# Performance work log

Measured on AMD Instinct MI355X. Metric: run time of the kernel, lower is better.

Reference implementation:

```python
import jax, jax.numpy as jnp
import numpy as np

NEG_SLOPE = 0.01  # torch leaky_relu default

def _lrelu(x):
    return jax.nn.leaky_relu(x, NEG_SLOPE)

def _l2norm(x, axis):
    # torch F.normalize(p=2, eps=1e-12)
    n = jnp.linalg.norm(x, axis=axis, keepdims=True)
    return x / jnp.maximum(n, 1e-12)

def setup_inputs() -> dict:
    key = jax.random.key(0)
    ks = jax.random.split(key, 12)
    Nda, Nq, C, Din, Dout = 10000, 64, 1024, 128, 256
    target_adj = (jax.random.uniform(ks[0], (Nda, Nda)) < 0.002).astype(jnp.float32)
    query_adj = (jax.random.uniform(ks[1], (Nq, Nq)) < 0.2).astype(jnp.float32)
    node_features_da = jax.random.normal(ks[2], (Nda, Din), dtype=jnp.float32)
    node_features_q = jax.random.normal(ks[3], (Nq, Din), dtype=jnp.float32)
    candidate_set = jax.random.randint(ks[4], (C,), 0, Nda)
    candidate_adj = (jax.random.uniform(ks[5], (C, C)) < 0.01).astype(jnp.float32)
    s_in = 1.0 / np.sqrt(Din).astype(np.float32)
    s_out = 1.0 / np.sqrt(Dout).astype(np.float32)
    W1_da = jax.random.normal(ks[6], (Din, Dout), dtype=jnp.float32) * s_in
    W1_q = jax.random.normal(ks[7], (Din, Dout), dtype=jnp.float32) * s_in
    W2_da = jax.random.normal(ks[8], (Dout, Dout), dtype=jnp.float32) * s_out
    W2_q = jax.random.normal(ks[9], (Dout, Dout), dtype=jnp.float32) * s_out
    threshold = jnp.float32(0.2)
    return {"target_adj": target_adj, "node_features_da": node_features_da,
            "query_adj": query_adj, "node_features_q": node_features_q,
            "candidate_set": candidate_set, "candidate_adj": candidate_adj,
            "threshold": threshold, "W1_da": W1_da, "W1_q": W1_q,
            "W2_da": W2_da, "W2_q": W2_q}

def _cross_cosine(q, da, candidate_set):
    # cosine similarity between each query node and each candidate target node: [Nq, C]
    return _l2norm(q, 1) @ _l2norm(da[candidate_set], 1).T

def reference(target_adj, node_features_da, query_adj, node_features_q,
              candidate_set, candidate_adj, threshold, W1_da, W1_q, W2_da, W2_q):
    # layer 1: GCN propagation on both graphs (gcn(adj,x) = adj @ x @ W)
    da1 = _lrelu(target_adj @ (node_features_da @ W1_da))   # [Nda, D]
    q1 = _lrelu(query_adj @ (node_features_q @ W1_q))       # [Nq, D]
    c1 = _cross_cosine(q1, da1, candidate_set)               # [Nq, C]
    pre_da1 = da1[candidate_set]                             # [C, D]
    # NOTE: da1[candidate_set].data = ... mutates a temporary in torch -> no-op on da1
    att_da1 = _lrelu(da1)                                    # dropout in eval = identity
    h1_q = c1 @ pre_da1                                      # [Nq, D]
    att_q1 = _lrelu(q1 + _l2norm(h1_q, 0))
    # layer 2
    da2 = _lrelu(target_adj @ (att_da1 @ W2_da))
    q2 = _lrelu(query_adj @ (att_q1 @ W2_q))
    c2 = _cross_cosine(q2, da2, candidate_set)
    pre_da2 = da2[candidate_set]
    att_da2 = _lrelu(da2)                                    # in-place update is again a no-op
    h2_q = c2 @ pre_da2
    att_q2 = _lrelu(q2 + _l2norm(h2_q, 0))
    # graph-level matching score per target node
    emb = jnp.mean(att_q2, axis=0, keepdims=True)            # [1, D]
    num = att_da2 @ emb[0]                                   # [Nda]
    den = jnp.maximum(jnp.linalg.norm(att_da2, axis=1) * jnp.linalg.norm(emb), 1e-8)
    end = (num / den)[None, :]                               # [1, Nda]
    # threshold selection expressed with a mask (jit-safe, same math: excluded
    # rows/cols are zero and do not affect L2 norms, sums, or the trace)
    m = (end[0] > threshold).astype(att_da2.dtype)           # [Nda]
    F_ = att_da2 * m[:, None]
    re_adj = F_ @ F_.T                                       # [Nda, Nda]
    nor_re = _l2norm(re_adj, 1) * target_adj                 # elementwise with original adj
    cnt = jnp.sum(m)
    total = jnp.sum(nor_re)
    tr = jnp.trace(nor_re)
    has = cnt > 0
    pre_avg_degree = jnp.where(has, total / jnp.maximum(cnt, 1.0), 0.0)
    pre_avg_nodes = jnp.where(has, tr, 0.0)
    pre_density = jnp.where(has, 2.0 * total / (tr * (tr - 1.0) + 1e-4), 0.0)
    return (end, att_da2, att_q2, pre_avg_degree, pre_density, pre_avg_nodes)
```

## Files before the change

kernel.cpp:

```cpp
#include <hip/hip_runtime.h>

constexpr int NDA = 10000;
constexpr int NQ  = 64;
constexpr int CND = 1024;
constexpr int DIN = 128;
constexpr int D   = 256;
constexpr int CAP = 96;
constexpr int NT128 = (NDA + 127) / 128;
constexpr int NB128 = NT128 * 2;
constexpr int NCHUNK = 32;
constexpr int GCHUNK = 320;

#define LRELU(x) ((x) >= 0.f ? (x) : 0.01f * (x))

__device__ __forceinline__ float wave_red64(float v) {
#pragma unroll
    for (int o = 32; o; o >>= 1) v += __shfl_down(v, o);
    return v;
}

struct GemmSmem    { float As[32][65]; float Bs[32][68]; };
struct Gemm128Smem { float As[16][132]; float Bs[16][132]; };
struct CrossSmem   { float qs[D]; float cmw[256]; int sci[256]; float red[4]; float sqn; float part[4][256]; };
struct SpmmSmem    { int sc[CAP]; float part[4][256]; };
struct CsrSmem     { int scnt; };
struct EndSmem     { float se[D]; float scnt; float red[4]; };
struct FinalSmem   { int sc[CAP]; float part[4][256]; int n; int sdiag; float r1[4], r2[4], r3[4]; };
struct Attq4Smem   { float hbuf[64][65]; float red[4][64]; float invs[64]; };

template <bool RELU_A, bool RELU_C>
__device__ __forceinline__ void gemm_body(GemmSmem& sm, int bx, int by,
                                          const float* __restrict__ A,
                                          const float* __restrict__ B,
                                          float* __restrict__ C,
                                          int M, int N, int K) {
    const int bm = bx * 64, bn = by * 64;
    const int tid = threadIdx.x;
    const int tx = tid & 15, ty = tid >> 4;
    const int lm = tid >> 2, lk = (tid & 3) * 8;
    const int kb = tid >> 3, nb = (tid & 7) * 8;
    const bool aValid = (bm + lm) < M;
    const float* aPtr = A + (size_t)(bm + lm) * K + lk;
    const float* bPtr = B + (size_t)kb * N + bn + nb;
    float4 ra0 = make_float4(0.f, 0.f, 0.f, 0.f), ra1 = ra0, rb0, rb1;
    if (aValid) { ra0 = *(const float4*)aPtr; ra1 = *(const float4*)(aPtr + 4); }
    rb0 = *(const float4*)bPtr;
    rb1 = *(const float4*)(bPtr + 4);
    float acc[4][4] = {};
    for (int k0 = 0; k0 < K; k0 += 32) {
        float4 wa0 = ra0, wa1 = ra1, wb0 = rb0, wb1 = rb1;
        if (RELU_A) {
            wa0.x = LRELU(wa0.x); wa0.y = LRELU(wa0.y); wa0.z = LRELU(wa0.z); wa0.w = LRELU(wa0.w);
            wa1.x = LRELU(wa1.x); wa1.y = LRELU(wa1.y); wa1.z = LRELU(wa1.z); wa1.w = LRELU(wa1.w);
        }
        sm.As[lk + 0][lm] = wa0.x; sm.As[lk + 1][lm] = wa0.y;
        sm.As[lk + 2][lm] = wa0.z; sm.As[lk + 3][lm] = wa0.w;
        sm.As[lk + 4][lm] = wa1.x; sm.As[lk + 5][lm] = wa1.y;
        sm.As[lk + 6][lm] = wa1.z; sm.As[lk + 7][lm] = wa1.w;
        *(float4*)&sm.Bs[kb][nb]     = wb0;
        *(float4*)&sm.Bs[kb][nb + 4] = wb1;
        __syncthreads();
        if (k0 + 32 < K) {
            if (aValid) {
                ra0 = *(const float4*)(aPtr + k0 + 32);
                ra1 = *(const float4*)(aPtr + k0 + 36);
            }
            rb0 = *(const float4*)(bPtr + (size_t)(k0 + 32) * N);
            rb1 = *(const float4*)(bPtr + (size_t)(k0 + 32) * N + 4);
        }
#pragma unroll
        for (int kk = 0; kk < 32; kk++) {
            float av[4], bv[4];
#pragma unroll
            for (int i = 0; i < 4; i++) av[i] = sm.As[kk][ty * 4 + i];
#pragma unroll
            for (int j = 0; j < 4; j++) bv[j] = sm.Bs[kk][tx * 4 + j];
#pragma unroll
            for (int i = 0; i < 4; i++)
#pragma unroll
                for (int j = 0; j < 4; j++) acc[i][j] += av[i] * bv[j];
        }
        __syncthreads();
    }
#pragma unroll
    for (int i = 0; i < 4; i++) {
        int r = bm + ty * 4 + i;
        if (r < M) {
            float4 v = make_float4(acc[i][0], acc[i][1], acc[i][2], acc[i][3]);
            if (RELU_C) { v.x = LRELU(v.x); v.y = LRELU(v.y); v.z = LRELU(v.z); v.w = LRELU(v.w); }
            *(float4*)(C + (size_t)r * N + bn + tx * 4) = v;
        }
    }
}

template <bool RELU_A>
__device__ __forceinline__ void gemm128_body(Gemm128Smem& sm, int bx, int by,
                                             const float* __restrict__ A,
                                             const float* __restrict__ B,
                                             float* __restrict__ C,
                                             int M, int N, int K) {
    const int bm = bx * 128, bn = by * 128;
    const int tid = threadIdx.x;
    const int tx = tid & 15, ty = tid >> 4;
    const int am = tid >> 1, ak = (tid & 1) * 8;
    const int bk = tid >> 4, bn8 = (tid & 15) * 8;
    const bool aValid = (bm + am) < M;
    const float* aPtr = A + (size_t)(bm + am) * K + ak;
    const float* bPtr = B + (size_t)bk * N + bn + bn8;
    float4 ra0 = make_float4(0.f, 0.f, 0.f, 0.f), ra1 = ra0, rb0, rb1;
    if (aValid) { ra0 = *(const float4*)aPtr; ra1 = *(const float4*)(aPtr + 4); }
    rb0 = *(const float4*)bPtr;
    rb1 = *(const float4*)(bPtr + 4);
    float acc[8][8] = {};
    for (int k0 = 0; k0 < K; k0 += 16) {
        float a8[8] = { ra0.x, ra0.y, ra0.z, ra0.w, ra1.x, ra1.y, ra1.z, ra1.w };
        if (RELU_A) {
#pragma unroll
            for (int j = 0; j < 8; j++) a8[j] = LRELU(a8[j]);
        }
#pragma unroll
        for (int j = 0; j < 8; j++) sm.As[ak + j][am] = a8[j];
        *(float4*)&sm.Bs[bk][bn8]     = rb0;
        *(float4*)&sm.Bs[bk][bn8 + 4] = rb1;
        __syncthreads();
        if (k0 + 16 < K) {
            if (aValid) {
                ra0 = *(const float4*)(aPtr + k0 + 16);
                ra1 = *(const float4*)(aPtr + k0 + 20);
            }
            rb0 = *(const float4*)(bPtr + (size_t)(k0 + 16) * N);
            rb1 = *(const float4*)(bPtr + (size_t)(k0 + 16) * N + 4);
        }
#pragma unroll
        for (int kk = 0; kk < 16; kk++) {
            float4 a0 = *(const float4*)&sm.As[kk][ty * 8];
            float4 a1 = *(const float4*)&sm.As[kk][ty * 8 + 4];
            float4 b0 = *(const float4*)&sm.Bs[kk][tx * 8];
            float4 b1 = *(const float4*)&sm.Bs[kk][tx * 8 + 4];
            float av[8] = { a0.x, a0.y, a0.z, a0.w, a1.x, a1.y, a1.z, a1.w };
            float bv[8] = { b0.x, b0.y, b0.z, b0.w, b1.x, b1.y, b1.z, b1.w };
#pragma unroll
            for (int i = 0; i < 8; i++)
#pragma unroll
                for (int j = 0; j < 8; j++) acc[i][j] += av[i] * bv[j];
        }
        __syncthreads();
    }
#pragma unroll
    for (int i = 0; i < 8; i++) {
        int r = bm + ty * 8 + i;
        if (r < M) {
            float4 v0 = make_float4(acc[i][0], acc[i][1], acc[i][2], acc[i][3]);
            float4 v1 = make_float4(acc[i][4], acc[i][5], acc[i][6], acc[i][7]);
            *(float4*)(C + (size_t)r * N + bn + tx * 8)     = v0;
            *(float4*)(C + (size_t)r * N + bn + tx * 8 + 4) = v1;
        }
    }
}

__device__ __forceinline__ void csr_body(CsrSmem& sm, const float* __restrict__ adj,
                                         int* __restrict__ cols,
                                         int* __restrict__ rowcnt, int row) {
    if (threadIdx.x == 0) sm.scnt = 0;
    __syncthreads();
    const float4* rp = (const float4*)(adj + (size_t)row * NDA);
    for (int i = threadIdx.x; i < NDA / 4; i += 256) {
        float4 v = rp[i];
        if (v.x != 0.f) { int s = atomicAdd(&sm.scnt, 1); if (s < CAP) cols[row * CAP + s] = 4 * i; }
        if (v.y != 0.f) { int s = atomicAdd(&sm.scnt, 1); if (s < CAP) cols[row * CAP + s] = 4 * i + 1; }
        if (v.z != 0.f) { int s = atomicAdd(&sm.scnt, 1); if (s < CAP) cols[row * CAP + s] = 4 * i + 2; }
        if (v.w != 0.f) { int s = atomicAdd(&sm.scnt, 1); if (s < CAP) cols[row * CAP + s] = 4 * i + 3; }
    }
    __syncthreads();
    if (threadIdx.x == 0) rowcnt[row] = min(sm.scnt, CAP);
}

__device__ __forceinline__ void spmm_body(SpmmSmem& sm, const int* __restrict__ cols,
                                          const int* __restrict__ rowcnt,
                                          const float* __restrict__ X,
                                          float* __restrict__ out1,
                                          float* __restrict__ out2, int row) {
    int t = threadIdx.x;
    int w = t >> 6, lane = t & 63;
    int cnt = rowcnt[row];
    if (t < cnt) sm.sc[t] = cols[row * CAP + t];
    __syncthreads();
    float4 acc = make_float4(0.f, 0.f, 0.f, 0.f);
    int k = w;
    for (; k + 4 < cnt; k += 8) {
        const float4* x0 = (const float4*)(X + (size_t)sm.sc[k] * D);
        const float4* x1 = (const float4*)(X + (size_t)sm.sc[k + 4] * D);
        float4 v0 = x0[lane];
        float4 v1 = x1[lane];
        acc.x += v0.x + v1.x; acc.y += v0.y + v1.y;
        acc.z += v0.z + v1.z; acc.w += v0.w + v1.w;
    }
    for (; k < cnt; k += 4) {
        const float4* x0 = (const float4*)(X + (size_t)sm.sc[k] * D);
        float4 v0 = x0[lane];
        acc.x += v0.x; acc.y += v0.y; acc.z += v0.z; acc.w += v0.w;
    }
    *(float4*)&sm.part[w][lane * 4] = acc;
    __syncthreads();
    float s = sm.part[0][t] + sm.part[1][t] + sm.part[2][t] + sm.part[3][t];
    float v = LRELU(s);
    out1[(size_t)row * D + t] = v;
    if (out2) out2[(size_t)row * D + t] = LRELU(v);
}

__device__ __forceinline__ void cross_body(CrossSmem& sm, const float* __restrict__ q,
                                           const float* __restrict__ da,
                                           const int* __restrict__ cand,
                                           float* __restrict__ hpart,
                                           int r, int qr) {
    int t = threadIdx.x;
    int w = t >> 6, lane = t & 63;
    float qv = q[r * D + t];
    sm.qs[t] = qv;
    sm.sci[t] = cand[qr * 256 + t];
    float p = wave_red64(qv * qv);
    if (lane == 0) sm.red[w] = p;
    __syncthreads();
    if (t == 0) sm.sqn = fmaxf(sqrtf(sm.red[0] + sm.red[1] + sm.red[2] + sm.red[3]), 1e-12f);
    __syncthreads();
    float qn = sm.sqn;
    float4 qv4 = *(const float4*)&sm.qs[lane * 4];
    for (int c = w * 64; c < w * 64 + 64; c++) {
        const float4* rp = (const float4*)(da + (size_t)sm.sci[c] * D);
        float4 v = rp[lane];
        float dp = qv4.x * v.x + qv4.y * v.y + qv4.z * v.z + qv4.w * v.w;
        float sq = v.x * v.x + v.y * v.y + v.z * v.z + v.w * v.w;
#pragma unroll
        for (int o = 32; o; o >>= 1) { dp += __shfl_down(dp, o); sq += __shfl_down(sq, o); }
        if (lane == 0) sm.cmw[c] = dp / (qn * fmaxf(sqrtf(sq), 1e-12f));
    }
    __syncthreads();
    float4 acc = make_float4(0.f, 0.f, 0.f, 0.f);
    for (int c = w; c < 256; c += 8) {
        float w0 = sm.cmw[c], w1 = sm.cmw[c + 4];
        const float4* p0 = (const float4*)(da + (size_t)sm.sci[c] * D);
        const float4* p1 = (const float4*)(da + (size_t)sm.sci[c + 4] * D);
        float4 v0 = p0[lane];
        float4 v1 = p1[lane];
        acc.x += w0 * v0.x + w1 * v1.x;
        acc.y += w0 * v0.y + w1 * v1.y;
        acc.z += w0 * v0.z + w1 * v1.z;
        acc.w += w0 * v0.w + w1 * v1.w;
    }
    *(float4*)&sm.part[w][lane * 4] = acc;
    __syncthreads();
    float hs = sm.part[0][t] + sm.part[1][t] + sm.part[2][t] + sm.part[3][t];
    hpart[((size_t)qr * NQ + r) * D + t] = hs;
}

__global__ __launch_bounds__(256) void stage0_kernel(const float* __restrict__ adj,
                                                     int* __restrict__ cols,
                                                     int* __restrict__ rowcnt,
                                                     const float* __restrict__ Fda,
                                                     const float* __restrict__ W1da,
                                                     float* __restrict__ X1,
                                                     const float* __restrict__ Fq,
                                                     const float* __restrict__ W1q,
                                                     float* __restrict__ Xq) {
    __shared__ union { Gemm128Smem h; GemmSmem g; CsrSmem z; } sm;
    int bid = blockIdx.x;
    if (bid < NB128) {
        gemm128_body<false>(sm.h, bid >> 1, bid & 1, Fda, W1da, X1, NDA, D, DIN);
    } else if (bid < NB128 + 4) {
        gemm_body<false, false>(sm.g, 0, bid - NB128, Fq, W1q, Xq, NQ, D, DIN);
    } else {
        csr_body(sm.z, adj, cols, rowcnt, bid - (NB128 + 4));
    }
}

__global__ __launch_bounds__(256) void stage_sg_kernel(const int* __restrict__ cols,
                                                       const int* __restrict__ rowcnt,
                                                       const float* __restrict__ X,
                                                       float* __restrict__ out1,
                                                       float* __restrict__ out2,
                                                       const float* __restrict__ Aq,
                                                       const float* __restrict__ Bq,
                                                       float* __restrict__ Cq) {
    __shared__ union { GemmSmem g; SpmmSmem s; } sm;
    int bid = blockIdx.x;
    if (bid < 4) {
        gemm_body<false, true>(sm.g, 0, bid, Aq, Bq, Cq, NQ, D, NQ);
    } else {
        spmm_body(sm.s, cols, rowcnt, X, out1, out2, bid - 4);
    }
}

__global__ __launch_bounds__(256) void mergeA_kernel(const float* __restrict__ q1,
                                                     const float* __restrict__ da1,
                                                     const int* __restrict__ cand,
                                                     float* __restrict__ hpart,
                                                     const float* __restrict__ W2da,
                                                     float* __restrict__ Y2) {
    __shared__ union { CrossSmem c; Gemm128Smem h; } sm;
    int bid = blockIdx.x;
    if (bid < 256) {
        cross_body(sm.c, q1, da1, cand, hpart, bid >> 2, bid & 3);
    } else {
        int t = bid - 256;
        gemm128_body<true>(sm.h, t >> 1, t & 1, da1, W2da, Y2, NDA, D, D);
    }
}

__global__ __launch_bounds__(256) void cross_kernel(const float* __restrict__ q,
                                                    const float* __restrict__ da,
                                                    const int* __restrict__ cand,
                                                    float* __restrict__ hpart) {
    __shared__ CrossSmem sm;
    cross_body(sm, q, da, cand, hpart, blockIdx.x, blockIdx.y);
}

__global__ __launch_bounds__(256) void qfused_kernel(const float* __restrict__ q,
                                                     const float* __restrict__ hpart,
                                                     const float* __restrict__ W2q,
                                                     float* __restrict__ Zq) {
    __shared__ float aqT[D][65];
    __shared__ float Bs[32][68];
    int d = threadIdx.x;
    float hv[NQ];
    float ss = 0.f;
#pragma unroll
    for (int r = 0; r < NQ; r++) {
        float h = hpart[(size_t)r * D + d]
                + hpart[(size_t)(NQ + r) * D + d]
                + hpart[(size_t)(2 * NQ + r) * D + d]
                + hpart[(size_t)(3 * NQ + r) * D + d];
        hv[r] = h;
        ss += h * h;
    }
    float inv = 1.f / fmaxf(sqrtf(ss), 1e-12f);
#pragma unroll
    for (int r = 0; r < NQ; r++) {
        float v = q[r * D + d] + hv[r] * inv;
        aqT[d][r] = LRELU(v);
    }
    __syncthreads();
    const int bn = blockIdx.x * 64;
    const int tx = d & 15, ty = d >> 4;
    const int kb = d >> 3, nb = (d & 7) * 8;
    float acc[4][4] = {};
    for (int k0 = 0; k0 < D; k0 += 32) {
        float4 b0 = *(const float4*)(W2q + (size_t)(k0 + kb) * D + bn + nb);
        float4 b1 = *(const float4*)(W2q + (size_t)(k0 + kb) * D + bn + nb + 4);
        *(float4*)&Bs[kb][nb]     = b0;
        *(float4*)&Bs[kb][nb + 4] = b1;
        __syncthreads();
#pragma unroll
        for (int kk = 0; kk < 32; kk++) {
            float av[4], bv[4];
#pragma unroll
            for (int i = 0; i < 4; i++) av[i] = aqT[k0 + kk][ty * 4 + i];
#pragma unroll
            for (int j = 0; j < 4; j++) bv[j] = Bs[kk][tx * 4 + j];
#pragma unroll
            for (int i = 0; i < 4; i++)
#pragma unroll
                for (int j = 0; j < 4; j++) acc[i][j] += av[i] * bv[j];
        }
        __syncthreads();
    }
#pragma unroll
    for (int i = 0; i < 4; i++) {
        float4 v = make_float4(acc[i][0], acc[i][1], acc[i][2], acc[i][3]);
        *(float4*)(Zq + (size_t)(ty * 4 + i) * D + bn + tx * 4) = v;
    }
}

__global__ __launch_bounds__(256) void attq4_kernel(const float* __restrict__ q,
                                                    const float* __restrict__ hpart,
                                                    float* __restrict__ attq,
                                                    float* __restrict__ emb,
                                                    float* __restrict__ cnt,
                                                    double* __restrict__ tot,
                                                    double* __restrict__ tr) {
    __shared__ Attq4Smem sm;
    int b = blockIdx.x, t = threadIdx.x;
    int lc = t & 63, rq = t >> 6;
    int c = b * 64 + lc;
    if (b == 0 && t == 0) { *cnt = 0.f; *tot = 0.0; *tr = 0.0; }
    float ss = 0.f;
#pragma unroll
    for (int rr = 0; rr < 16; rr++) {
        int r = rq * 16 + rr;
        float h = hpart[(size_t)r * D + c]
                + hpart[(size_t)(NQ + r) * D + c]
                + hpart[(size_t)(2 * NQ + r) * D + c]
                + hpart[(size_t)(3 * NQ + r) * D + c];
        sm.hbuf[r][lc] = h;
        ss += h * h;
    }
    sm.red[rq][lc] = ss;
    __syncthreads();
    if (rq == 0) {
        float s = sm.red[0][lc] + sm.red[1][lc] + sm.red[2][lc] + sm.red[3][lc];
        sm.invs[lc] = 1.f / fmaxf(sqrtf(s), 1e-12f);
    }
    __syncthreads();
    float inv = sm.invs[lc];
    float es = 0.f;
#pragma unroll
    for (int rr = 0; rr < 16; rr++) {
        int r = rq * 16 + rr;
        float v = q[r * D + c] + sm.hbuf[r][lc] * inv;
        v = LRELU(v);
        attq[r * D + c] = v;
        es += v;
    }
    __syncthreads();
    sm.red[rq][lc] = es;
    __syncthreads();
    if (rq == 0) {
        float e = (sm.red[0][lc] + sm.red[1][lc] + sm.red[2][lc] + sm.red[3][lc]) * (1.f / (float)NQ);
        emb[c] = e;
    }
}

__global__ __launch_bounds__(256) void end_kernel(const float* __restrict__ A,
                                                  const float* __restrict__ emb,
                                                  const float* __restrict__ thr_p,
                                                  float* __restrict__ endv,
                                                  float* __restrict__ m,
                                                  float* __restrict__ cnt) {
    __shared__ EndSmem sm;
    int d = threadIdx.x;
    float ev = emb[d];
    sm.se[d] = ev;
    if (d == 0) sm.scnt = 0.f;
    int w = d >> 6, lane = d & 63;
    float pe = wave_red64(ev * ev);
    if (lane == 0) sm.red[w] = pe;
    __syncthreads();
    float embn = sqrtf(sm.red[0] + sm.red[1] + sm.red[2] + sm.red[3]);
    float thr = *thr_p;
    int row = blockIdx.x * 4 + w;
    const float* ar = A + (size_t)row * D;
    float num = 0.f, sq = 0.f;
#pragma unroll
    for (int s = 0; s < 4; s++) {
        float v = ar[lane + 64 * s];
        num += v * sm.se[lane + 64 * s];
        sq += v * v;
    }
#pragma unroll
    for (int o = 32; o; o >>= 1) { num += __shfl_down(num, o); sq += __shfl_down(sq, o); }
    if (lane == 0) {
        float den = fmaxf(sqrtf(sq) * embn, 1e-8f);
        float e = num / den;
        endv[row] = e;
        float mv = e > thr ? 1.f : 0.f;
        m[row] = mv;
        if (mv != 0.f) atomicAdd(&sm.scnt, 1.f);
    }
    __syncthreads();
    if (d == 0 && sm.scnt != 0.f) atomicAdd(cnt, sm.scnt);
}

__global__ __launch_bounds__(256) void Gpart_kernel(const float* __restrict__ A,
                                                    const float* __restrict__ m,
                                                    float* __restrict__ Gp) {
    __shared__ Gemm128Smem sm;
    int ti = blockIdx.x >> 1, tj = blockIdx.x & 1;
    int base = blockIdx.y * GCHUNK;
    int tid = threadIdx.x;
    int tx = tid & 15, ty = tid >> 4;
    int sr = tid >> 4, sc8 = (tid & 15) * 8;
    float acc[8][8] = {};
    for (int g0 = 0; g0 < GCHUNK; g0 += 16) {
        int r = base + g0 + sr;
        float4 va0 = make_float4(0.f, 0.f, 0.f, 0.f), va1 = va0, vb0 = va0, vb1 = va0;
        float mv = 0.f;
        if (r < NDA) {
            mv = m[r];
            const float* ar = A + (size_t)r * D;
            va0 = *(const float4*)(ar + ti * 128 + sc8);
            va1 = *(const float4*)(ar + ti * 128 + sc8 + 4);
            vb0 = *(const float4*)(ar + tj * 128 + sc8);
            vb1 = *(const float4*)(ar + tj * 128 + sc8 + 4);
        }
        va0.x *= mv; va0.y *= mv; va0.z *= mv; va0.w *= mv;
        va1.x *= mv; va1.y *= mv; va1.z *= mv; va1.w *= mv;
        *(float4*)&sm.As[sr][sc8]     = va0;
        *(float4*)&sm.As[sr][sc8 + 4] = va1;
        *(float4*)&sm.Bs[sr][sc8]     = vb0;
        *(float4*)&sm.Bs[sr][sc8 + 4] = vb1;
        __syncthreads();
#pragma unroll
        for (int kk = 0; kk < 16; kk++) {
            float4 a0 = *(const float4*)&sm.As[kk][ty * 8];
            float4 a1 = *(const float4*)&sm.As[kk][ty * 8 + 4];
            float4 b0 = *(const float4*)&sm.Bs[kk][tx * 8];
            float4 b1 = *(const float4*)&sm.Bs[kk][tx * 8 + 4];
            float av[8] = { a0.x, a0.y, a0.z, a0.w, a1.x, a1.y, a1.z, a1.w };
            float bv[8] = { b0.x, b0.y, b0.z, b0.w, b1.x, b1.y, b1.z, b1.w };
#pragma unroll
            for (int i = 0; i < 8; i++)
#pragma unroll
                for (int j = 0; j < 8; j++) acc[i][j] += av[i] * bv[j];
        }
        __syncthreads();
    }
    float* gp = Gp + (size_t)blockIdx.y * D * D;
#pragma unroll
    for (int i = 0; i < 8; i++) {
        int gi = ti * 128 + ty * 8 + i;
        float4 v0 = make_float4(acc[i][0], acc[i][1], acc[i][2], acc[i][3]);
        float4 v1 = make_float4(acc[i][4], acc[i][5], acc[i][6], acc[i][7]);
        *(float4*)(gp + (size_t)gi * D + tj * 128 + tx * 8)     = v0;
        *(float4*)(gp + (size_t)gi * D + tj * 128 + tx * 8 + 4) = v1;
    }
}

__global__ __launch_bounds__(256) void Gred_kernel(const float* __restrict__ Gp,
                                                   float* __restrict__ G) {
    int idx = blockIdx.x * 256 + threadIdx.x;
    float s = 0.f;
#pragma unroll
    for (int c = 0; c < NCHUNK; c++) s += Gp[(size_t)c * D * D + idx];
    G[idx] = s;
}

__global__ __launch_bounds__(256) void gemmH_kernel(const float* __restrict__ A,
                                                    const float* __restrict__ B,
                                                    float* __restrict__ C) {
    __shared__ Gemm128Smem sm;
    gemm128_body<false>(sm, blockIdx.x >> 1, blockIdx.x & 1, A, B, C, NDA, D, D);
}

__global__ __launch_bounds__(256) void final_kernel(const int* __restrict__ cols,
                                                    const int* __restrict__ rowcnt,
                                                    const float* __restrict__ m,
                                                    const float* __restrict__ A,
                                                    const float* __restrict__ H,
                                                    double* __restrict__ total,
                                                    double* __restrict__ tr) {
    int i = blockIdx.x;
    if (m[i] == 0.f) return;
    __shared__ FinalSmem sm;
    int t = threadIdx.x;
    int w = t >> 6, lane = t & 63;
    int cnt = rowcnt[i];
    if (t == 0) { sm.n = 0; sm.sdiag = 0; }
    __syncthreads();
    if (t < cnt) {
        int j = cols[i * CAP + t];
        if (m[j] != 0.f) {
            int s = atomicAdd(&sm.n, 1);
            sm.sc[s] = j;
            if (j == i) sm.sdiag = 1;
        }
    }
    __syncthreads();
    int n = sm.n;
    float4 acc = make_float4(0.f, 0.f, 0.f, 0.f);
    int k = w;
    for (; k + 4 < n; k += 8) {
        const float4* x0 = (const float4*)(A + (size_t)sm.sc[k] * D);
        const float4* x1 = (const float4*)(A + (size_t)sm.sc[k + 4] * D);
        float4 v0 = x0[lane];
        float4 v1 = x1[lane];
        acc.x += v0.x + v1.x; acc.y += v0.y + v1.y;
        acc.z += v0.z + v1.z; acc.w += v0.w + v1.w;
    }
    for (; k < n; k += 4) {
        const float4* x0 = (const float4*)(A + (size_t)sm.sc[k] * D);
        float4 v0 = x0[lane];
        acc.x += v0.x; acc.y += v0.y; acc.z += v0.z; acc.w += v0.w;
    }
    *(float4*)&sm.part[w][lane * 4] = acc;
    __syncthreads();
    float av = A[(size_t)i * D + t];
    float hv = H[(size_t)i * D + t];
    float sd = sm.part[0][t] + sm.part[1][t] + sm.part[2][t] + sm.part[3][t];
    float p1 = av * sd, p2 = av * hv, p3 = av * av;
#pragma unroll
    for (int o = 32; o; o >>= 1) {
        p1 += __shfl_down(p1, o);
        p2 += __shfl_down(p2, o);
        p3 += __shfl_down(p3, o);
    }
    if (lane == 0) { sm.r1[w] = p1; sm.r2[w] = p2; sm.r3[w] = p3; }
    __syncthreads();
    if (t == 0) {
        float num  = sm.r1[0] + sm.r1[1] + sm.r1[2] + sm.r1[3];
        float den2 = sm.r2[0] + sm.r2[1] + sm.r2[2] + sm.r2[3];
        float self = sm.r3[0] + sm.r3[1] + sm.r3[2] + sm.r3[3];
        float denom = fmaxf(sqrtf(den2), 1e-12f);
        double inv = 1.0 / (double)denom;
        if (num != 0.f) atomicAdd(total, (double)num * inv);
        if (sm.sdiag) atomicAdd(tr, (double)self * inv);
    }
}

__global__ void scalars_kernel(const float* __restrict__ cnt,
                               const double* __restrict__ total,
                               const double* __restrict__ tr,
                               float* __restrict__ out) {
    float c = *cnt;
    float T = (float)*total;
    float R = (float)*tr;
    bool has = c > 0.f;
    out[0] = has ? (T / fmaxf(c, 1.f)) : 0.f;
    out[1] = has ? (2.f * T / (R * (R - 1.f) + 1e-4f)) : 0.f;
    out[2] = has ? R : 0.f;
}

extern "C" void kernel_launch(void* const* d_in, const int* in_sizes, int n_in,
                              void* d_out, int out_size, void* d_ws, size_t ws_size,
                              hipStream_t stream) {
    (void)in_sizes; (void)n_in; (void)out_size; (void)ws_size;
    const float* adj  = (const float*)d_in[0];
    const float* Fda  = (const float*)d_in[1];
    const float* Qadj = (const float*)d_in[2];
    const float* Fq   = (const float*)d_in[3];
    const int*   cand = (const int*)d_in[4];
    const float* thr  = (const float*)d_in[6];
    const float* W1da = (const float*)d_in[7];
    const float* W1q  = (const float*)d_in[8];
    const float* W2da = (const float*)d_in[9];
    const float* W2q  = (const float*)d_in[10];

    float* out = (float*)d_out;
    float* o_end    = out;
    float* o_attda2 = out + NDA;
    float* o_attq2  = out + NDA + (size_t)NDA * D;
    float* o_sc     = o_attq2 + NQ * D;

    char* w = (char*)d_ws;
    size_t off = 0;
    auto alloc = [&](size_t b) { size_t r = off; off += (b + 255) & ~(size_t)255; return r; };
    float* bufA = (float*)(w + alloc((size_t)NDA * D * 4));
    float* bufB = (float*)(w + alloc((size_t)NDA * D * 4));
    float* bufC = (float*)(w + alloc((size_t)NDA * D * 4));
    int* colsb   = (int*)(w + alloc((size_t)NDA * CAP * 4));
    int* rowcntb = (int*)(w + alloc((size_t)NDA * 4));
    float* mbuf  = (float*)(w + alloc((size_t)NDA * 4));
    float* Gb    = (float*)(w + alloc((size_t)D * D * 4));
    float* Gp    = (float*)(w + alloc((size_t)NCHUNK * D * D * 4));
    char* zbase = w + alloc(256);
    float* cntb  = (float*)zbase;
    double* totb = (double*)(zbase + 8);
    double* trb  = (double*)(zbase + 16);
    float* xq   = (float*)(w + alloc((size_t)NQ * D * 4));
    float* q1b  = (float*)(w + alloc((size_t)NQ * D * 4));
    float* q2b  = (float*)(w + alloc((size_t)NQ * D * 4));
    float* hpart = (float*)(w + alloc((size_t)4 * NQ * D * 4));
    float* embb = (float*)(w + alloc((size_t)(D + 1) * 4));

    stage0_kernel<<<NB128 + 4 + NDA, 256, 0, stream>>>(adj, colsb, rowcntb,
                                                       Fda, W1da, bufA, Fq, W1q, xq);
    stage_sg_kernel<<<NDA + 4, 256, 0, stream>>>(colsb, rowcntb, bufA, bufB, (float*)nullptr,
                                                 Qadj, xq, q1b);
    mergeA_kernel<<<256 + NB128, 256, 0, stream>>>(q1b, bufB, cand, hpart, W2da, bufA);
    qfused_kernel<<<4, 256, 0, stream>>>(q1b, hpart, W2q, xq);
    stage_sg_kernel<<<NDA + 4, 256, 0, stream>>>(colsb, rowcntb, bufA, bufC, o_attda2,
                                                 Qadj, xq, q2b);
    cross_kernel<<<dim3(NQ, 4), 256, 0, stream>>>(q2b, bufC, cand, hpart);
    attq4_kernel<<<4, 256, 0, stream>>>(q2b, hpart, o_attq2, embb, cntb, totb, trb);
    end_kernel<<<NDA / 4, 256, 0, stream>>>(o_attda2, embb, thr, o_end, mbuf, cntb);
    Gpart_kernel<<<dim3(4, NCHUNK), 256, 0, stream>>>(o_attda2, mbuf, Gp);
    Gred_kernel<<<D * D / 256, 256, 0, stream>>>(Gp, Gb);
    gemmH_kernel<<<NB128, 256, 0, stream>>>(o_attda2, Gb, bufB);
    final_kernel<<<NDA, 256, 0, stream>>>(colsb, rowcntb, mbuf, o_attda2, bufB, totb, trb);
    scalars_kernel<<<1, 1, 0, stream>>>(cntb, totb, trb, o_sc);
}
```

Before: 1.096 ms.

## Replace 128-tile GEMMs with 64-tile GEMMs and atomic Gram accumulation

Removes the 128x128 register-blocked GEMM body and switches every dense Nda-by-256 GEMM (layer-1 projection, W2 projection, the H multiply) to the existing 64x64 tile kernel, which launches more blocks. The Gram matrix F^T F is now computed by a simpler 64x64-tile kernel with 8-row smem staging. Partial results go straight into G via float atomics, dropping the partial buffer and the separate reduction kernel. G is zeroed inside stage0 through extra blocks. The cost is lower register reuse per thread, many atomics on a 256x256 buffer, and nondeterministic summation order.

```diff
diff --git a/kernel.cpp b/kernel.cpp
--- a/kernel.cpp
+++ b/kernel.cpp
@@ -6,10 +6,8 @@
 constexpr int DIN = 128;
 constexpr int D   = 256;
 constexpr int CAP = 96;
-constexpr int NT128 = (NDA + 127) / 128;
-constexpr int NB128 = NT128 * 2;
-constexpr int NCHUNK = 32;
-constexpr int GCHUNK = 320;
+constexpr int NB64 = ((NDA + 63) / 64) * (D / 64);
+constexpr int GCHUNK = 400;
 
 #define LRELU(x) ((x) >= 0.f ? (x) : 0.01f * (x))
 
@@ -19,14 +17,13 @@
     return v;
 }
 
-struct GemmSmem    { float As[32][65]; float Bs[32][68]; };
-struct Gemm128Smem { float As[16][132]; float Bs[16][132]; };
-struct CrossSmem   { float qs[D]; float cmw[256]; int sci[256]; float red[4]; float sqn; float part[4][256]; };
-struct SpmmSmem    { int sc[CAP]; float part[4][256]; };
-struct CsrSmem     { int scnt; };
-struct EndSmem     { float se[D]; float scnt; float red[4]; };
-struct FinalSmem   { int sc[CAP]; float part[4][256]; int n; int sdiag; float r1[4], r2[4], r3[4]; };
-struct Attq4Smem   { float hbuf[64][65]; float red[4][64]; float invs[64]; };
+struct GemmSmem  { float As[32][65]; float Bs[32][68]; };
+struct CrossSmem { float qs[D]; float cmw[256]; int sci[256]; float red[4]; float sqn; float part[4][256]; };
+struct SpmmSmem  { int sc[CAP]; float part[4][256]; };
+struct CsrSmem   { int scnt; };
+struct EndSmem   { float se[D]; float scnt; float red[4]; };
+struct FinalSmem { int sc[CAP]; float part[4][256]; int n; int sdiag; float r1[4], r2[4], r3[4]; };
+struct Attq4Smem { float hbuf[64][65]; float red[4][64]; float invs[64]; };
 
 template <bool RELU_A, bool RELU_C>
 __device__ __forceinline__ void gemm_body(GemmSmem& sm, int bx, int by,
@@ -93,71 +90,6 @@
     }
 }
 
-template <bool RELU_A>
-__device__ __forceinline__ void gemm128_body(Gemm128Smem& sm, int bx, int by,
-                                             const float* __restrict__ A,
-                                             const float* __restrict__ B,
-                                             float* __restrict__ C,
-                                             int M, int N, int K) {
-    const int bm = bx * 128, bn = by * 128;
-    const int tid = threadIdx.x;
-    const int tx = tid & 15, ty = tid >> 4;
-    const int am = tid >> 1, ak = (tid & 1) * 8;
-    const int bk = tid >> 4, bn8 = (tid & 15) * 8;
-    const bool aValid = (bm + am) < M;
-    const float* aPtr = A + (size_t)(bm + am) * K + ak;
-    const float* bPtr = B + (size_t)bk * N + bn + bn8;
-    float4 ra0 = make_float4(0.f, 0.f, 0.f, 0.f), ra1 = ra0, rb0, rb1;
-    if (aValid) { ra0 = *(const float4*)aPtr; ra1 = *(const float4*)(aPtr + 4); }
-    rb0 = *(const float4*)bPtr;
-    rb1 = *(const float4*)(bPtr + 4);
-    float acc[8][8] = {};
-    for (int k0 = 0; k0 < K; k0 += 16) {
-        float a8[8] = { ra0.x, ra0.y, ra0.z, ra0.w, ra1.x, ra1.y, ra1.z, ra1.w };
-        if (RELU_A) {
-#pragma unroll
-            for (int j = 0; j < 8; j++) a8[j] = LRELU(a8[j]);
-        }
-#pragma unroll
-        for (int j = 0; j < 8; j++) sm.As[ak + j][am] = a8[j];
-        *(float4*)&sm.Bs[bk][bn8]     = rb0;
-        *(float4*)&sm.Bs[bk][bn8 + 4] = rb1;
-        __syncthreads();
-        if (k0 + 16 < K) {
-            if (aValid) {
-                ra0 = *(const float4*)(aPtr + k0 + 16);
-                ra1 = *(const float4*)(aPtr + k0 + 20);
-            }
-            rb0 = *(const float4*)(bPtr + (size_t)(k0 + 16) * N);
-            rb1 = *(const float4*)(bPtr + (size_t)(k0 + 16) * N + 4);
-        }
-#pragma unroll
-        for (int kk = 0; kk < 16; kk++) {
-            float4 a0 = *(const float4*)&sm.As[kk][ty * 8];
-            float4 a1 = *(const float4*)&sm.As[kk][ty * 8 + 4];
-            float4 b0 = *(const float4*)&sm.Bs[kk][tx * 8];
-            float4 b1 = *(const float4*)&sm.Bs[kk][tx * 8 + 4];
-            float av[8] = { a0.x, a0.y, a0.z, a0.w, a1.x, a1.y, a1.z, a1.w };
-            float bv[8] = { b0.x, b0.y, b0.z, b0.w, b1.x, b1.y, b1.z, b1.w };
-#pragma unroll
-            for (int i = 0; i < 8; i++)
-#pragma unroll
-                for (int j = 0; j < 8; j++) acc[i][j] += av[i] * bv[j];
-        }
-        __syncthreads();
-    }
-#pragma unroll
-    for (int i = 0; i < 8; i++) {
-        int r = bm + ty * 8 + i;
-        if (r < M) {
-            float4 v0 = make_float4(acc[i][0], acc[i][1], acc[i][2], acc[i][3]);
-            float4 v1 = make_float4(acc[i][4], acc[i][5], acc[i][6], acc[i][7]);
-            *(float4*)(C + (size_t)r * N + bn + tx * 8)     = v0;
-            *(float4*)(C + (size_t)r * N + bn + tx * 8 + 4) = v1;
-        }
-    }
-}
-
 __device__ __forceinline__ void csr_body(CsrSmem& sm, const float* __restrict__ adj,
                                          int* __restrict__ cols,
                                          int* __restrict__ rowcnt, int row) {
@@ -261,15 +193,23 @@
                                                      float* __restrict__ X1,
                                                      const float* __restrict__ Fq,
                                                      const float* __restrict__ W1q,
-                                                     float* __restrict__ Xq) {
-    __shared__ union { Gemm128Smem h; GemmSmem g; CsrSmem z; } sm;
+                                                     float* __restrict__ Xq,
+                                                     float* __restrict__ G) {
+    __shared__ union { GemmSmem g; CsrSmem z; } sm;
     int bid = blockIdx.x;
-    if (bid < NB128) {
-        gemm128_body<false>(sm.h, bid >> 1, bid & 1, Fda, W1da, X1, NDA, D, DIN);
-    } else if (bid < NB128 + 4) {
-        gemm_body<false, false>(sm.g, 0, bid - NB128, Fq, W1q, Xq, NQ, D, DIN);
+    if (bid < NB64) {
+        gemm_body<false, false>(sm.g, bid >> 2, bid & 3, Fda, W1da, X1, NDA, D, DIN);
+    } else if (bid < NB64 + 4) {
+        gemm_body<false, false>(sm.g, 0, bid - NB64, Fq, W1q, Xq, NQ, D, DIN);
+    } else if (bid < NB64 + 20) {
+        int zb = bid - (NB64 + 4);
+        float4* g4 = (float4*)G;
+        int base = zb * 1024 + threadIdx.x;
+#pragma unroll
+        for (int k = 0; k < 4; k++)
+            g4[base + k * 256] = make_float4(0.f, 0.f, 0.f, 0.f);
     } else {
-        csr_body(sm.z, adj, cols, rowcnt, bid - (NB128 + 4));
+        csr_body(sm.z, adj, cols, rowcnt, bid - (NB64 + 20));
     }
 }
 
@@ -296,13 +236,13 @@
                                                      float* __restrict__ hpart,
                                                      const float* __restrict__ W2da,
                                                      float* __restrict__ Y2) {
-    __shared__ union { CrossSmem c; Gemm128Smem h; } sm;
+    __shared__ union { CrossSmem c; GemmSmem g; } sm;
     int bid = blockIdx.x;
     if (bid < 256) {
         cross_body(sm.c, q1, da1, cand, hpart, bid >> 2, bid & 3);
     } else {
         int t = bid - 256;
-        gemm128_body<true>(sm.h, t >> 1, t & 1, da1, W2da, Y2, NDA, D, D);
+        gemm_body<true, false>(sm.g, t >> 2, t & 3, da1, W2da, Y2, NDA, D, D);
     }
 }
 
@@ -459,75 +399,50 @@
     if (d == 0 && sm.scnt != 0.f) atomicAdd(cnt, sm.scnt);
 }
 
-__global__ __launch_bounds__(256) void Gpart_kernel(const float* __restrict__ A,
-                                                    const float* __restrict__ m,
-                                                    float* __restrict__ Gp) {
-    __shared__ Gemm128Smem sm;
-    int ti = blockIdx.x >> 1, tj = blockIdx.x & 1;
+__global__ __launch_bounds__(256) void G_kernel(const float* __restrict__ A,
+                                                const float* __restrict__ m,
+                                                float* __restrict__ G) {
+    __shared__ float SA[8][64], SB[8][64];
+    int ti = blockIdx.x >> 2, tj = blockIdx.x & 3;
     int base = blockIdx.y * GCHUNK;
     int tid = threadIdx.x;
     int tx = tid & 15, ty = tid >> 4;
-    int sr = tid >> 4, sc8 = (tid & 15) * 8;
-    float acc[8][8] = {};
-    for (int g0 = 0; g0 < GCHUNK; g0 += 16) {
-        int r = base + g0 + sr;
-        float4 va0 = make_float4(0.f, 0.f, 0.f, 0.f), va1 = va0, vb0 = va0, vb1 = va0;
-        float mv = 0.f;
-        if (r < NDA) {
-            mv = m[r];
-            const float* ar = A + (size_t)r * D;
-            va0 = *(const float4*)(ar + ti * 128 + sc8);
-            va1 = *(const float4*)(ar + ti * 128 + sc8 + 4);
-            vb0 = *(const float4*)(ar + tj * 128 + sc8);
-            vb1 = *(const float4*)(ar + tj * 128 + sc8 + 4);
-        }
-        va0.x *= mv; va0.y *= mv; va0.z *= mv; va0.w *= mv;
-        va1.x *= mv; va1.y *= mv; va1.z *= mv; va1.w *= mv;
-        *(float4*)&sm.As[sr][sc8]     = va0;
-        *(float4*)&sm.As[sr][sc8 + 4] = va1;
-        *(float4*)&sm.Bs[sr][sc8]     = vb0;
-        *(float4*)&sm.Bs[sr][sc8 + 4] = vb1;
+    float acc[4][4] = {};
+    for (int g0 = 0; g0 < GCHUNK; g0 += 8) {
+        for (int l = tid; l < 512; l += 256) {
+            int rr = l >> 6, c = l & 63;
+            int r = base + g0 + rr;
+            float mv = m[r];
+            SA[rr][c] = A[(size_t)r * D + ti * 64 + c] * mv;
+            SB[rr][c] = A[(size_t)r * D + tj * 64 + c];
+        }
         __syncthreads();
 #pragma unroll
-        for (int kk = 0; kk < 16; kk++) {
-            float4 a0 = *(const float4*)&sm.As[kk][ty * 8];
-            float4 a1 = *(const float4*)&sm.As[kk][ty * 8 + 4];
-            float4 b0 = *(const float4*)&sm.Bs[kk][tx * 8];
-            float4 b1 = *(const float4*)&sm.Bs[kk][tx * 8 + 4];
-            float av[8] = { a0.x, a0.y, a0.z, a0.w, a1.x, a1.y, a1.z, a1.w };
-            float bv[8] = { b0.x, b0.y, b0.z, b0.w, b1.x, b1.y, b1.z, b1.w };
-#pragma unroll
-            for (int i = 0; i < 8; i++)
-#pragma unroll
-                for (int j = 0; j < 8; j++) acc[i][j] += av[i] * bv[j];
+        for (int rr = 0; rr < 8; rr++) {
+            float av[4], bv[4];
+#pragma unroll
+            for (int i = 0; i < 4; i++) av[i] = SA[rr][ty * 4 + i];
+#pragma unroll
+            for (int j = 0; j < 4; j++) bv[j] = SB[rr][tx * 4 + j];
+#pragma unroll
+            for (int i = 0; i < 4; i++)
+#pragma unroll
+                for (int j = 0; j < 4; j++) acc[i][j] += av[i] * bv[j];
         }
         __syncthreads();
     }
-    float* gp = Gp + (size_t)blockIdx.y * D * D;
-#pragma unroll
-    for (int i = 0; i < 8; i++) {
-        int gi = ti * 128 + ty * 8 + i;
-        float4 v0 = make_float4(acc[i][0], acc[i][1], acc[i][2], acc[i][3]);
-        float4 v1 = make_float4(acc[i][4], acc[i][5], acc[i][6], acc[i][7]);
-        *(float4*)(gp + (size_t)gi * D + tj * 128 + tx * 8)     = v0;
-        *(float4*)(gp + (size_t)gi * D + tj * 128 + tx * 8 + 4) = v1;
-    }
-}
-
-__global__ __launch_bounds__(256) void Gred_kernel(const float* __restrict__ Gp,
-                                                   float* __restrict__ G) {
-    int idx = blockIdx.x * 256 + threadIdx.x;
-    float s = 0.f;
-#pragma unroll
-    for (int c = 0; c < NCHUNK; c++) s += Gp[(size_t)c * D * D + idx];
-    G[idx] = s;
+#pragma unroll
+    for (int i = 0; i < 4; i++)
+#pragma unroll
+        for (int j = 0; j < 4; j++)
+            atomicAdd(&G[(ti * 64 + ty * 4 + i) * D + tj * 64 + tx * 4 + j], acc[i][j]);
 }
 
 __global__ __launch_bounds__(256) void gemmH_kernel(const float* __restrict__ A,
                                                     const float* __restrict__ B,
                                                     float* __restrict__ C) {
-    __shared__ Gemm128Smem sm;
-    gemm128_body<false>(sm, blockIdx.x >> 1, blockIdx.x & 1, A, B, C, NDA, D, D);
+    __shared__ GemmSmem sm;
+    gemm_body<false, false>(sm, blockIdx.x, blockIdx.y, A, B, C, NDA, D, D);
 }
 
 __global__ __launch_bounds__(256) void final_kernel(const int* __restrict__ cols,
@@ -639,7 +554,6 @@
     int* rowcntb = (int*)(w + alloc((size_t)NDA * 4));
     float* mbuf  = (float*)(w + alloc((size_t)NDA * 4));
     float* Gb    = (float*)(w + alloc((size_t)D * D * 4));
-    float* Gp    = (float*)(w + alloc((size_t)NCHUNK * D * D * 4));
     char* zbase = w + alloc(256);
     float* cntb  = (float*)zbase;
     double* totb = (double*)(zbase + 8);
@@ -650,20 +564,19 @@
     float* hpart = (float*)(w + alloc((size_t)4 * NQ * D * 4));
     float* embb = (float*)(w + alloc((size_t)(D + 1) * 4));
 
-    stage0_kernel<<<NB128 + 4 + NDA, 256, 0, stream>>>(adj, colsb, rowcntb,
-                                                       Fda, W1da, bufA, Fq, W1q, xq);
+    stage0_kernel<<<NB64 + 20 + NDA, 256, 0, stream>>>(adj, colsb, rowcntb,
+                                                       Fda, W1da, bufA, Fq, W1q, xq, Gb);
     stage_sg_kernel<<<NDA + 4, 256, 0, stream>>>(colsb, rowcntb, bufA, bufB, (float*)nullptr,
                                                  Qadj, xq, q1b);
-    mergeA_kernel<<<256 + NB128, 256, 0, stream>>>(q1b, bufB, cand, hpart, W2da, bufA);
+    mergeA_kernel<<<256 + NB64, 256, 0, stream>>>(q1b, bufB, cand, hpart, W2da, bufA);
     qfused_kernel<<<4, 256, 0, stream>>>(q1b, hpart, W2q, xq);
     stage_sg_kernel<<<NDA + 4, 256, 0, stream>>>(colsb, rowcntb, bufA, bufC, o_attda2,
                                                  Qadj, xq, q2b);
     cross_kernel<<<dim3(NQ, 4), 256, 0, stream>>>(q2b, bufC, cand, hpart);
     attq4_kernel<<<4, 256, 0, stream>>>(q2b, hpart, o_attq2, embb, cntb, totb, trb);
     end_kernel<<<NDA / 4, 256, 0, stream>>>(o_attda2, embb, thr, o_end, mbuf, cntb);
-    Gpart_kernel<<<dim3(4, NCHUNK), 256, 0, stream>>>(o_attda2, mbuf, Gp);
-    Gred_kernel<<<D * D / 256, 256, 0, stream>>>(Gp, Gb);
-    gemmH_kernel<<<NB128, 256, 0, stream>>>(o_attda2, Gb, bufB);
+    G_kernel<<<dim3(16, NDA / GCHUNK), 256, 0, stream>>>(o_attda2, mbuf, Gb);
+    gemmH_kernel<<<dim3((NDA + 63) / 64, D / 64), 256, 0, stream>>>(o_attda2, Gb, bufB);
     final_kernel<<<NDA, 256, 0, stream>>>(colsb, rowcntb, mbuf, o_attda2, bufB, totb, trb);
     scalars_kernel<<<1, 1, 0, stream>>>(cntb, totb, trb, o_sc);
 }
```

Result: no change. 1.078 ms (-1.7%).
